# Kernel optimization log

Hardware: AMD Instinct MI355X
Metric: run time of the kernel (lower is better)

Reference implementation:

```python
import jax, jax.numpy as jnp
import numpy as np

N = 100000
E = 1600000
IN_DIM = 512
HID = 64
OUT = 2


def gcn_conv(x, src, dst, W, b, n):
    # transform first (PyG GCNConv: x = x @ W, then propagate)
    xt = x @ W  # [n, d_out]
    # add self-loops
    loop = jnp.arange(n, dtype=src.dtype)
    src_sl = jnp.concatenate([src, loop])
    dst_sl = jnp.concatenate([dst, loop])
    # symmetric normalization: deg over destination (col) incl. self-loops
    ones = jnp.ones(src_sl.shape[0], dtype=xt.dtype)
    deg = jax.ops.segment_sum(ones, dst_sl, num_segments=n)
    dis = jnp.where(deg > 0, jax.lax.rsqrt(deg), 0.0)  # deg^-1/2, inf -> 0
    norm = dis[src_sl] * dis[dst_sl]  # [E+n]
    msgs = xt[src_sl] * norm[:, None]  # gather + scale
    out = jax.ops.segment_sum(msgs, dst_sl, num_segments=n)  # scatter-add
    return out + b


def setup_inputs() -> dict:
    key = jax.random.key(0)
    k0, k1, k2, k3, k4, k5 = jax.random.split(key, 6)
    x = jax.random.normal(k0, (N, IN_DIM), dtype=jnp.float32)
    edge_index = jax.random.randint(k1, (2, E), 0, N, dtype=jnp.int64)
    s1 = 1.0 / np.sqrt(IN_DIM)
    s2 = 1.0 / np.sqrt(HID)
    W1 = jax.random.uniform(k2, (IN_DIM, HID), jnp.float32, -s1, s1)
    b1 = jax.random.uniform(k3, (HID,), jnp.float32, -s1, s1)
    W2 = jax.random.uniform(k4, (HID, OUT), jnp.float32, -s2, s2)
    b2 = jax.random.uniform(k5, (OUT,), jnp.float32, -s2, s2)
    return {"x": x, "edge_index": edge_index, "W1": W1, "b1": b1, "W2": W2, "b2": b2}


def reference(x, edge_index, W1, b1, W2, b2):
    src, dst = edge_index[0], edge_index[1]
    h = gcn_conv(x, src, dst, W1, b1, N)
    h = jax.nn.relu(h)
    # dropout is identity in eval mode (training=False)
    h = gcn_conv(h, src, dst, W2, b2, N)
    return jax.nn.log_softmax(h, axis=1)
```

## Files before the change

### kernel.cpp

```cpp
#include <hip/hip_runtime.h>
#include <hip/hip_bf16.h>

#define NN 100000
#define EE 1600000
#define IN_DIM 512
#define HID 64
#define NB1 391
#define NCH 196
#define CHUNK 8192
#define NGEMM 1563
#define ARENA 5120
#define GA 800
#define GB (NGEMM - GA)

typedef __attribute__((ext_vector_type(8))) short bf16x8;
typedef __attribute__((ext_vector_type(4))) float f32x4;

static __device__ __forceinline__ short f2bf(float f) {
    __hip_bfloat16 h = __float2bfloat16(f);
    return *reinterpret_cast<short*>(&h);
}
static __device__ __forceinline__ float bf2f(unsigned short u) {
    union { unsigned int i; float f; } c; c.i = ((unsigned int)u) << 16;
    return c.f;
}

__device__ __forceinline__ void do_gemm(int gb, const float* __restrict__ x,
                                        const bf16x8* __restrict__ W1p,
                                        unsigned short* __restrict__ xt1b) {
    const int wave = threadIdx.x >> 6;
    const int lane = threadIdx.x & 63;
    const int r = lane & 15;
    const int kg = lane >> 4;
    const int row0 = gb * 64 + wave * 16;
    const int rowc = min(row0 + r, NN - 1);
    const float* xr = x + (size_t)rowc * IN_DIM;

    f32x4 acc[4] = {};
#pragma unroll
    for (int ks = 0; ks < 16; ++ks) {
        const int k0 = ks * 32 + kg * 8;
        float4 xa = *(const float4*)(xr + k0);
        float4 xb = *(const float4*)(xr + k0 + 4);
        bf16x8 a;
        a[0] = f2bf(xa.x); a[1] = f2bf(xa.y); a[2] = f2bf(xa.z); a[3] = f2bf(xa.w);
        a[4] = f2bf(xb.x); a[5] = f2bf(xb.y); a[6] = f2bf(xb.z); a[7] = f2bf(xb.w);
        const int bbase = (ks * 4 + kg) * 64;
#pragma unroll
        for (int cb = 0; cb < 4; ++cb) {
            bf16x8 bfr = W1p[bbase + cb * 16 + r];
            acc[cb] = __builtin_amdgcn_mfma_f32_16x16x32_bf16(a, bfr, acc[cb], 0, 0, 0);
        }
    }
#pragma unroll
    for (int cb = 0; cb < 4; ++cb) {
#pragma unroll
        for (int reg = 0; reg < 4; ++reg) {
            int ro = row0 + kg * 4 + reg;
            if (ro < NN) xt1b[(size_t)ro * HID + cb * 16 + r] =
                (unsigned short)f2bf(acc[cb][reg]);
        }
    }
}

__global__ __launch_bounds__(256) void pack_hist_kernel(const float* __restrict__ W1,
                                                        bf16x8* __restrict__ W1p,
                                                        const int* __restrict__ dst,
                                                        int* __restrict__ cnt2d) {
    if (blockIdx.x < 16) {
        int t = blockIdx.x * 256 + threadIdx.x;
        int kstep = t >> 8;
        int kb = (t >> 6) & 3;
        int col = t & 63;
        int kbase = kstep * 32 + kb * 8;
        bf16x8 v;
#pragma unroll
        for (int j = 0; j < 8; ++j) v[j] = f2bf(W1[(size_t)(kbase + j) * HID + col]);
        W1p[t] = v;
    } else {
        __shared__ int h[NB1];
        const int c = blockIdx.x - 16;
        const int t = threadIdx.x;
        for (int i = t; i < NB1; i += 256) h[i] = 0;
        __syncthreads();
        const int base = c * CHUNK;
        for (int i = t; i < CHUNK; i += 256) {
            int e = base + i;
            if (e < EE) atomicAdd(&h[dst[e] >> 8], 1);
        }
        __syncthreads();
        for (int i = t; i < NB1; i += 256) cnt2d[c * NB1 + i] = h[i];
    }
}

__global__ __launch_bounds__(256) void scatter_gemm_kernel(
        const int* __restrict__ src, const int* __restrict__ dst,
        const int* __restrict__ cnt2d, unsigned int* __restrict__ pairs,
        int* __restrict__ edge_cnt,
        const float* __restrict__ x, const bf16x8* __restrict__ W1p,
        unsigned short* __restrict__ xt1b) {
    if (blockIdx.x < NCH) {
        __shared__ int cur[NB1];
        const int c = blockIdx.x;
        const int t = threadIdx.x;
        for (int i = t; i < NB1; i += 256) {
            int run = 0, pp = 0;
            for (int c2 = 0; c2 < NCH; ++c2) {
                int v = cnt2d[c2 * NB1 + i];
                if (c2 == c) pp = run;
                run += v;
            }
            cur[i] = i * ARENA + pp;
            if (c == 0) edge_cnt[i] = run;
        }
        __syncthreads();
        const int base = c * CHUNK;
        for (int i = t; i < CHUNK; i += 256) {
            int e = base + i;
            if (e < EE) {
                int s = src[e], d = dst[e];
                int bkt = d >> 8;
                int pos = atomicAdd(&cur[bkt], 1);
                if (pos < (bkt + 1) * ARENA)
                    pairs[pos] = ((unsigned int)s << 8) | (unsigned int)(d & 255);
            }
        }
    } else {
        do_gemm(blockIdx.x - NCH, x, W1p, xt1b);
    }
}

__global__ __launch_bounds__(256) void sort_gemm_kernel(
        const unsigned int* __restrict__ pairs, const int* __restrict__ edge_cnt,
        int* __restrict__ offsets, int* __restrict__ cursor,
        int* __restrict__ sorted_src, float* __restrict__ dis,
        const float* __restrict__ x, const bf16x8* __restrict__ W1p,
        unsigned short* __restrict__ xt1b) {
    if (blockIdx.x < NB1) {
        __shared__ int sdeg[256];
        __shared__ int sinc[256];
        __shared__ int scur[256];
        const int b = blockIdx.x;
        const int t = threadIdx.x;
        const int n0 = b << 8;
        const int nn = min(256, NN - n0);
        const int e0 = b * ARENA;
        const int e1 = e0 + min(edge_cnt[b], ARENA);

        sdeg[t] = 0;
        __syncthreads();
        for (int e = e0 + t; e < e1; e += 256)
            atomicAdd(&sdeg[pairs[e] & 255u], 1);
        __syncthreads();
        sinc[t] = sdeg[t];
        __syncthreads();
        for (int off = 1; off < 256; off <<= 1) {
            int v = (t >= off) ? sinc[t - off] : 0;
            __syncthreads();
            sinc[t] += v;
            __syncthreads();
        }
        int excl = sinc[t] - sdeg[t];
        scur[t] = excl;
        if (t < nn) {
            offsets[n0 + t] = e0 + excl;
            cursor[n0 + t]  = e0 + excl + sdeg[t];
            dis[n0 + t]     = rsqrtf((float)sdeg[t] + 1.0f);
        }
        __syncthreads();
        for (int e = e0 + t; e < e1; e += 256) {
            unsigned int p = pairs[e];
            int pos = atomicAdd(&scur[p & 255u], 1);
            sorted_src[e0 + pos] = (int)(p >> 8);
        }
    } else {
        do_gemm(GA + (blockIdx.x - NB1), x, W1p, xt1b);
    }
}

__global__ __launch_bounds__(256) void agg1_fused_kernel(
        const int* __restrict__ offsets, const int* __restrict__ cursor,
        const int* __restrict__ sorted_src, const float* __restrict__ dis,
        const unsigned short* __restrict__ xt1b, const float* __restrict__ b1,
        const float* __restrict__ W2, float* __restrict__ xt2) {
    int node = blockIdx.x * 4 + (threadIdx.x >> 6);
    if (node >= NN) return;
    const int lane = threadIdx.x & 63;
    const int grp = lane >> 4;
    const int fl = lane & 15;
    const int beg = offsets[node], end = cursor[node];
    const float dd = dis[node];
    float acc0 = 0.f, acc1 = 0.f, acc2 = 0.f, acc3 = 0.f;

    for (int base = beg; base < end; base += 64) {
        int m = min(64, end - base);
        int s = 0;
        float nd = 0.f;
        if (lane < m) {
            s = sorted_src[base + lane];
            nd = dis[s];
        }
#pragma unroll 4
        for (int jj = 0; jj < m; jj += 4) {
            int j = jj + grp;
            int sj = __shfl(s, j);
            float nj = __shfl(nd, j);
            float w = (j < m) ? nj : 0.f;
            ushort4 v = *(const ushort4*)(xt1b + (size_t)sj * HID + fl * 4);
            acc0 += bf2f(v.x) * w;
            acc1 += bf2f(v.y) * w;
            acc2 += bf2f(v.z) * w;
            acc3 += bf2f(v.w) * w;
        }
    }
    acc0 += __shfl_xor(acc0, 16); acc0 += __shfl_xor(acc0, 32);
    acc1 += __shfl_xor(acc1, 16); acc1 += __shfl_xor(acc1, 32);
    acc2 += __shfl_xor(acc2, 16); acc2 += __shfl_xor(acc2, 32);
    acc3 += __shfl_xor(acc3, 16); acc3 += __shfl_xor(acc3, 32);

    ushort4 xs = *(const ushort4*)(xt1b + (size_t)node * HID + fl * 4);
    float4 bb = *(const float4*)(b1 + fl * 4);
    float d2 = dd * dd;
    float h0 = fmaxf(acc0 * dd + bf2f(xs.x) * d2 + bb.x, 0.f);
    float h1 = fmaxf(acc1 * dd + bf2f(xs.y) * d2 + bb.y, 0.f);
    float h2 = fmaxf(acc2 * dd + bf2f(xs.z) * d2 + bb.z, 0.f);
    float h3 = fmaxf(acc3 * dd + bf2f(xs.w) * d2 + bb.w, 0.f);

    float4 w01 = *(const float4*)(W2 + fl * 8);
    float4 w23 = *(const float4*)(W2 + fl * 8 + 4);
    float a0 = h0 * w01.x + h1 * w01.z + h2 * w23.x + h3 * w23.z;
    float a1 = h0 * w01.y + h1 * w01.w + h2 * w23.y + h3 * w23.w;
    a0 += __shfl_xor(a0, 1); a0 += __shfl_xor(a0, 2);
    a0 += __shfl_xor(a0, 4); a0 += __shfl_xor(a0, 8);
    a1 += __shfl_xor(a1, 1); a1 += __shfl_xor(a1, 2);
    a1 += __shfl_xor(a1, 4); a1 += __shfl_xor(a1, 8);
    if (lane == 0) *(float2*)(xt2 + (size_t)node * 2) = make_float2(a0, a1);
}

__global__ void agg2_final_kernel(const int* __restrict__ offsets, const int* __restrict__ cursor,
                                  const int* __restrict__ sorted_src,
                                  const float* __restrict__ dis,
                                  const float* __restrict__ xt2,
                                  const float* __restrict__ b2,
                                  float* __restrict__ out) {
    int node = blockIdx.x * 256 + threadIdx.x;
    if (node >= NN) return;
    int beg = offsets[node], end = cursor[node];
    float dd = dis[node];
    float d2 = dd * dd;
    float a0 = xt2[(size_t)node * 2 + 0] * d2;
    float a1 = xt2[(size_t)node * 2 + 1] * d2;
    for (int p = beg; p < end; ++p) {
        int s = sorted_src[p];
        float nrm = dis[s] * dd;
        float2 v = *(const float2*)(xt2 + (size_t)s * 2);
        a0 += v.x * nrm;
        a1 += v.y * nrm;
    }
    float v0 = a0 + b2[0], v1 = a1 + b2[1];
    float m = fmaxf(v0, v1);
    float lse = m + logf(expf(v0 - m) + expf(v1 - m));
    out[(size_t)node * 2 + 0] = v0 - lse;
    out[(size_t)node * 2 + 1] = v1 - lse;
}

extern "C" void kernel_launch(void* const* d_in, const int* in_sizes, int n_in,
                              void* d_out, int out_size, void* d_ws, size_t ws_size,
                              hipStream_t stream) {
    const float* x  = (const float*)d_in[0];
    const int* ei   = (const int*)d_in[1];
    const float* W1 = (const float*)d_in[2];
    const float* b1 = (const float*)d_in[3];
    const float* W2 = (const float*)d_in[4];
    const float* b2 = (const float*)d_in[5];
    const int* src = ei;
    const int* dst = ei + EE;
    float* out = (float*)d_out;

    unsigned short* xt1b = (unsigned short*)d_ws;
    float* dis        = (float*)(xt1b + (size_t)NN * HID);
    int*   offsets    = (int*)(dis + NN);
    int*   cursor     = offsets + NN;
    float* xt2        = (float*)(cursor + NN);
    bf16x8* W1p       = (bf16x8*)(xt2 + (size_t)NN * 2);
    int*   cnt2d      = (int*)(W1p + 4096);
    int*   edge_cnt   = cnt2d + NCH * NB1;
    int*   sorted_src = edge_cnt + NB1;
    unsigned int* pairs = (unsigned int*)(sorted_src + (size_t)NB1 * ARENA);

    pack_hist_kernel<<<16 + NCH, 256, 0, stream>>>(W1, W1p, dst, cnt2d);
    scatter_gemm_kernel<<<NCH + GA, 256, 0, stream>>>(src, dst, cnt2d, pairs, edge_cnt,
                                                      x, W1p, xt1b);
    sort_gemm_kernel<<<NB1 + GB, 256, 0, stream>>>(pairs, edge_cnt, offsets, cursor,
                                                   sorted_src, dis, x, W1p, xt1b);
    agg1_fused_kernel<<<(NN + 3) / 4, 256, 0, stream>>>(offsets, cursor, sorted_src,
                                                        dis, xt1b, b1, W2, xt2);
    agg2_final_kernel<<<(NN + 255) / 256, 256, 0, stream>>>(offsets, cursor, sorted_src,
                                                            dis, xt2, b2, out);
}
```

Baseline: 165.0 us.

## Fold degree normalization into GEMM output and fuse bucket sort with layer-1 aggregation

Result: slower. 322.9 us (+95.7%).

```diff
diff --git a/kernel.cpp b/kernel.cpp
--- a/kernel.cpp
+++ b/kernel.cpp
@@ -10,8 +10,6 @@
 #define CHUNK 8192
 #define NGEMM 1563
 #define ARENA 5120
-#define GA 800
-#define GB (NGEMM - GA)
 
 typedef __attribute__((ext_vector_type(8))) short bf16x8;
 typedef __attribute__((ext_vector_type(4))) float f32x4;
@@ -25,48 +23,11 @@
     return c.f;
 }
 
-__device__ __forceinline__ void do_gemm(int gb, const float* __restrict__ x,
-                                        const bf16x8* __restrict__ W1p,
-                                        unsigned short* __restrict__ xt1b) {
-    const int wave = threadIdx.x >> 6;
-    const int lane = threadIdx.x & 63;
-    const int r = lane & 15;
-    const int kg = lane >> 4;
-    const int row0 = gb * 64 + wave * 16;
-    const int rowc = min(row0 + r, NN - 1);
-    const float* xr = x + (size_t)rowc * IN_DIM;
-
-    f32x4 acc[4] = {};
-#pragma unroll
-    for (int ks = 0; ks < 16; ++ks) {
-        const int k0 = ks * 32 + kg * 8;
-        float4 xa = *(const float4*)(xr + k0);
-        float4 xb = *(const float4*)(xr + k0 + 4);
-        bf16x8 a;
-        a[0] = f2bf(xa.x); a[1] = f2bf(xa.y); a[2] = f2bf(xa.z); a[3] = f2bf(xa.w);
-        a[4] = f2bf(xb.x); a[5] = f2bf(xb.y); a[6] = f2bf(xb.z); a[7] = f2bf(xb.w);
-        const int bbase = (ks * 4 + kg) * 64;
-#pragma unroll
-        for (int cb = 0; cb < 4; ++cb) {
-            bf16x8 bfr = W1p[bbase + cb * 16 + r];
-            acc[cb] = __builtin_amdgcn_mfma_f32_16x16x32_bf16(a, bfr, acc[cb], 0, 0, 0);
-        }
-    }
-#pragma unroll
-    for (int cb = 0; cb < 4; ++cb) {
-#pragma unroll
-        for (int reg = 0; reg < 4; ++reg) {
-            int ro = row0 + kg * 4 + reg;
-            if (ro < NN) xt1b[(size_t)ro * HID + cb * 16 + r] =
-                (unsigned short)f2bf(acc[cb][reg]);
-        }
-    }
-}
-
 __global__ __launch_bounds__(256) void pack_hist_kernel(const float* __restrict__ W1,
                                                         bf16x8* __restrict__ W1p,
                                                         const int* __restrict__ dst,
-                                                        int* __restrict__ cnt2d) {
+                                                        int* __restrict__ cnt2d,
+                                                        int* __restrict__ deg) {
     if (blockIdx.x < 16) {
         int t = blockIdx.x * 256 + threadIdx.x;
         int kstep = t >> 8;
@@ -86,7 +47,11 @@
         const int base = c * CHUNK;
         for (int i = t; i < CHUNK; i += 256) {
             int e = base + i;
-            if (e < EE) atomicAdd(&h[dst[e] >> 8], 1);
+            if (e < EE) {
+                int d = dst[e];
+                atomicAdd(&h[d >> 8], 1);
+                atomicAdd(&deg[d], 1);
+            }
         }
         __syncthreads();
         for (int i = t; i < NB1; i += 256) cnt2d[c * NB1 + i] = h[i];
@@ -98,7 +63,8 @@
         const int* __restrict__ cnt2d, unsigned int* __restrict__ pairs,
         int* __restrict__ edge_cnt,
         const float* __restrict__ x, const bf16x8* __restrict__ W1p,
-        unsigned short* __restrict__ xt1b) {
+        const int* __restrict__ deg, float* __restrict__ dis,
+        unsigned short* __restrict__ y) {
     if (blockIdx.x < NCH) {
         __shared__ int cur[NB1];
         const int c = blockIdx.x;
@@ -126,142 +92,169 @@
             }
         }
     } else {
-        do_gemm(blockIdx.x - NCH, x, W1p, xt1b);
-    }
-}
-
-__global__ __launch_bounds__(256) void sort_gemm_kernel(
+        const int gb = blockIdx.x - NCH;
+        const int wave = threadIdx.x >> 6;
+        const int lane = threadIdx.x & 63;
+        const int r = lane & 15;
+        const int kg = lane >> 4;
+        const int row0 = gb * 64 + wave * 16;
+        const int rowc = min(row0 + r, NN - 1);
+        const float* xr = x + (size_t)rowc * IN_DIM;
+
+        f32x4 acc[4] = {};
+#pragma unroll
+        for (int ks = 0; ks < 16; ++ks) {
+            const int k0 = ks * 32 + kg * 8;
+            float4 xa = *(const float4*)(xr + k0);
+            float4 xb = *(const float4*)(xr + k0 + 4);
+            bf16x8 a;
+            a[0] = f2bf(xa.x); a[1] = f2bf(xa.y); a[2] = f2bf(xa.z); a[3] = f2bf(xa.w);
+            a[4] = f2bf(xb.x); a[5] = f2bf(xb.y); a[6] = f2bf(xb.z); a[7] = f2bf(xb.w);
+            const int bbase = (ks * 4 + kg) * 64;
+#pragma unroll
+            for (int cb = 0; cb < 4; ++cb) {
+                bf16x8 bfr = W1p[bbase + cb * 16 + r];
+                acc[cb] = __builtin_amdgcn_mfma_f32_16x16x32_bf16(a, bfr, acc[cb], 0, 0, 0);
+            }
+        }
+        float di[4];
+#pragma unroll
+        for (int reg = 0; reg < 4; ++reg) {
+            int ro = row0 + kg * 4 + reg;
+            di[reg] = (ro < NN) ? rsqrtf((float)deg[ro] + 1.0f) : 0.f;
+            if (r == 0 && ro < NN) dis[ro] = di[reg];
+        }
+#pragma unroll
+        for (int cb = 0; cb < 4; ++cb) {
+#pragma unroll
+            for (int reg = 0; reg < 4; ++reg) {
+                int ro = row0 + kg * 4 + reg;
+                if (ro < NN) y[(size_t)ro * HID + cb * 16 + r] =
+                    (unsigned short)f2bf(di[reg] * acc[cb][reg]);
+            }
+        }
+    }
+}
+
+__global__ __launch_bounds__(256) void sortagg1_kernel(
         const unsigned int* __restrict__ pairs, const int* __restrict__ edge_cnt,
-        int* __restrict__ offsets, int* __restrict__ cursor,
-        int* __restrict__ sorted_src, float* __restrict__ dis,
-        const float* __restrict__ x, const bf16x8* __restrict__ W1p,
-        unsigned short* __restrict__ xt1b) {
-    if (blockIdx.x < NB1) {
-        __shared__ int sdeg[256];
-        __shared__ int sinc[256];
-        __shared__ int scur[256];
-        const int b = blockIdx.x;
-        const int t = threadIdx.x;
-        const int n0 = b << 8;
-        const int nn = min(256, NN - n0);
-        const int e0 = b * ARENA;
-        const int e1 = e0 + min(edge_cnt[b], ARENA);
-
-        sdeg[t] = 0;
-        __syncthreads();
-        for (int e = e0 + t; e < e1; e += 256)
-            atomicAdd(&sdeg[pairs[e] & 255u], 1);
-        __syncthreads();
-        sinc[t] = sdeg[t];
-        __syncthreads();
-        for (int off = 1; off < 256; off <<= 1) {
-            int v = (t >= off) ? sinc[t - off] : 0;
-            __syncthreads();
-            sinc[t] += v;
-            __syncthreads();
-        }
-        int excl = sinc[t] - sdeg[t];
-        scur[t] = excl;
-        if (t < nn) {
-            offsets[n0 + t] = e0 + excl;
-            cursor[n0 + t]  = e0 + excl + sdeg[t];
-            dis[n0 + t]     = rsqrtf((float)sdeg[t] + 1.0f);
-        }
-        __syncthreads();
-        for (int e = e0 + t; e < e1; e += 256) {
-            unsigned int p = pairs[e];
-            int pos = atomicAdd(&scur[p & 255u], 1);
-            sorted_src[e0 + pos] = (int)(p >> 8);
-        }
-    } else {
-        do_gemm(GA + (blockIdx.x - NB1), x, W1p, xt1b);
-    }
-}
-
-__global__ __launch_bounds__(256) void agg1_fused_kernel(
-        const int* __restrict__ offsets, const int* __restrict__ cursor,
-        const int* __restrict__ sorted_src, const float* __restrict__ dis,
-        const unsigned short* __restrict__ xt1b, const float* __restrict__ b1,
-        const float* __restrict__ W2, float* __restrict__ xt2) {
-    int node = blockIdx.x * 4 + (threadIdx.x >> 6);
-    if (node >= NN) return;
-    const int lane = threadIdx.x & 63;
+        const unsigned short* __restrict__ y, const float* __restrict__ b1,
+        const float* __restrict__ W2, float* __restrict__ z) {
+    __shared__ int lds_src[ARENA];
+    __shared__ int sdeg[256];
+    __shared__ int sinc[256];
+    __shared__ int scur[256];
+    const int b = blockIdx.x;
+    const int t = threadIdx.x;
+    const int n0 = b << 8;
+    const int e0 = b * ARENA;
+    const int cnt = min(edge_cnt[b], ARENA);
+
+    sdeg[t] = 0;
+    __syncthreads();
+    for (int e = t; e < cnt; e += 256)
+        atomicAdd(&sdeg[pairs[e0 + e] & 255u], 1);
+    __syncthreads();
+    sinc[t] = sdeg[t];
+    __syncthreads();
+    for (int off = 1; off < 256; off <<= 1) {
+        int v = (t >= off) ? sinc[t - off] : 0;
+        __syncthreads();
+        sinc[t] += v;
+        __syncthreads();
+    }
+    scur[t] = sinc[t] - sdeg[t];
+    __syncthreads();
+    for (int e = t; e < cnt; e += 256) {
+        unsigned int p = pairs[e0 + e];
+        int pos = atomicAdd(&scur[p & 255u], 1);
+        lds_src[pos] = (int)(p >> 8);
+    }
+    __syncthreads();
+
+    const int w = t >> 6;
+    const int lane = t & 63;
     const int grp = lane >> 4;
     const int fl = lane & 15;
-    const int beg = offsets[node], end = cursor[node];
-    const float dd = dis[node];
-    float acc0 = 0.f, acc1 = 0.f, acc2 = 0.f, acc3 = 0.f;
-
-    for (int base = beg; base < end; base += 64) {
-        int m = min(64, end - base);
-        int s = 0;
-        float nd = 0.f;
-        if (lane < m) {
-            s = sorted_src[base + lane];
-            nd = dis[s];
-        }
-#pragma unroll 4
-        for (int jj = 0; jj < m; jj += 4) {
+    const float4 bb = *(const float4*)(b1 + fl * 4);
+    const float4 w01 = *(const float4*)(W2 + fl * 8);
+    const float4 w23 = *(const float4*)(W2 + fl * 8 + 4);
+
+    for (int i = 0; i < 64; ++i) {
+        int n = w * 64 + i;
+        int node = n0 + n;
+        if (node >= NN) break;
+        int len = sdeg[n];
+        int beg = sinc[n] - len;
+        float dd = rsqrtf((float)len + 1.0f);
+        float acc0 = 0.f, acc1 = 0.f, acc2 = 0.f, acc3 = 0.f;
+        if (grp == 0) {
+            ushort4 v = *(const ushort4*)(y + (size_t)node * HID + fl * 4);
+            acc0 = bf2f(v.x); acc1 = bf2f(v.y); acc2 = bf2f(v.z); acc3 = bf2f(v.w);
+        }
+        for (int jj = 0; jj < len; jj += 4) {
             int j = jj + grp;
-            int sj = __shfl(s, j);
-            float nj = __shfl(nd, j);
-            float w = (j < m) ? nj : 0.f;
-            ushort4 v = *(const ushort4*)(xt1b + (size_t)sj * HID + fl * 4);
-            acc0 += bf2f(v.x) * w;
-            acc1 += bf2f(v.y) * w;
-            acc2 += bf2f(v.z) * w;
-            acc3 += bf2f(v.w) * w;
-        }
-    }
-    acc0 += __shfl_xor(acc0, 16); acc0 += __shfl_xor(acc0, 32);
-    acc1 += __shfl_xor(acc1, 16); acc1 += __shfl_xor(acc1, 32);
-    acc2 += __shfl_xor(acc2, 16); acc2 += __shfl_xor(acc2, 32);
-    acc3 += __shfl_xor(acc3, 16); acc3 += __shfl_xor(acc3, 32);
-
-    ushort4 xs = *(const ushort4*)(xt1b + (size_t)node * HID + fl * 4);
-    float4 bb = *(const float4*)(b1 + fl * 4);
-    float d2 = dd * dd;
-    float h0 = fmaxf(acc0 * dd + bf2f(xs.x) * d2 + bb.x, 0.f);
-    float h1 = fmaxf(acc1 * dd + bf2f(xs.y) * d2 + bb.y, 0.f);
-    float h2 = fmaxf(acc2 * dd + bf2f(xs.z) * d2 + bb.z, 0.f);
-    float h3 = fmaxf(acc3 * dd + bf2f(xs.w) * d2 + bb.w, 0.f);
-
-    float4 w01 = *(const float4*)(W2 + fl * 8);
-    float4 w23 = *(const float4*)(W2 + fl * 8 + 4);
-    float a0 = h0 * w01.x + h1 * w01.z + h2 * w23.x + h3 * w23.z;
-    float a1 = h0 * w01.y + h1 * w01.w + h2 * w23.y + h3 * w23.w;
-    a0 += __shfl_xor(a0, 1); a0 += __shfl_xor(a0, 2);
-    a0 += __shfl_xor(a0, 4); a0 += __shfl_xor(a0, 8);
-    a1 += __shfl_xor(a1, 1); a1 += __shfl_xor(a1, 2);
-    a1 += __shfl_xor(a1, 4); a1 += __shfl_xor(a1, 8);
-    if (lane == 0) *(float2*)(xt2 + (size_t)node * 2) = make_float2(a0, a1);
-}
-
-__global__ void agg2_final_kernel(const int* __restrict__ offsets, const int* __restrict__ cursor,
-                                  const int* __restrict__ sorted_src,
-                                  const float* __restrict__ dis,
-                                  const float* __restrict__ xt2,
-                                  const float* __restrict__ b2,
-                                  float* __restrict__ out) {
-    int node = blockIdx.x * 256 + threadIdx.x;
-    if (node >= NN) return;
-    int beg = offsets[node], end = cursor[node];
-    float dd = dis[node];
-    float d2 = dd * dd;
-    float a0 = xt2[(size_t)node * 2 + 0] * d2;
-    float a1 = xt2[(size_t)node * 2 + 1] * d2;
-    for (int p = beg; p < end; ++p) {
-        int s = sorted_src[p];
-        float nrm = dis[s] * dd;
-        float2 v = *(const float2*)(xt2 + (size_t)s * 2);
-        a0 += v.x * nrm;
-        a1 += v.y * nrm;
-    }
-    float v0 = a0 + b2[0], v1 = a1 + b2[1];
-    float m = fmaxf(v0, v1);
-    float lse = m + logf(expf(v0 - m) + expf(v1 - m));
-    out[(size_t)node * 2 + 0] = v0 - lse;
-    out[(size_t)node * 2 + 1] = v1 - lse;
+            if (j < len) {
+                int s = lds_src[beg + j];
+                ushort4 v = *(const ushort4*)(y + (size_t)s * HID + fl * 4);
+                acc0 += bf2f(v.x);
+                acc1 += bf2f(v.y);
+                acc2 += bf2f(v.z);
+                acc3 += bf2f(v.w);
+            }
+        }
+        acc0 += __shfl_xor(acc0, 16); acc0 += __shfl_xor(acc0, 32);
+        acc1 += __shfl_xor(acc1, 16); acc1 += __shfl_xor(acc1, 32);
+        acc2 += __shfl_xor(acc2, 16); acc2 += __shfl_xor(acc2, 32);
+        acc3 += __shfl_xor(acc3, 16); acc3 += __shfl_xor(acc3, 32);
+
+        float h0 = fmaxf(acc0 * dd + bb.x, 0.f);
+        float h1 = fmaxf(acc1 * dd + bb.y, 0.f);
+        float h2 = fmaxf(acc2 * dd + bb.z, 0.f);
+        float h3 = fmaxf(acc3 * dd + bb.w, 0.f);
+
+        float a0 = h0 * w01.x + h1 * w01.z + h2 * w23.x + h3 * w23.z;
+        float a1 = h0 * w01.y + h1 * w01.w + h2 * w23.y + h3 * w23.w;
+        a0 += __shfl_xor(a0, 1); a0 += __shfl_xor(a0, 2);
+        a0 += __shfl_xor(a0, 4); a0 += __shfl_xor(a0, 8);
+        a1 += __shfl_xor(a1, 1); a1 += __shfl_xor(a1, 2);
+        a1 += __shfl_xor(a1, 4); a1 += __shfl_xor(a1, 8);
+        if (lane == 0) *(float2*)(z + (size_t)node * 2) = make_float2(dd * a0, dd * a1);
+    }
+}
+
+__global__ __launch_bounds__(256) void agg2_kernel(
+        const unsigned int* __restrict__ pairs, const int* __restrict__ edge_cnt,
+        const float* __restrict__ dis, const float* __restrict__ z,
+        const float* __restrict__ b2, float* __restrict__ out) {
+    __shared__ float acc2[256][2];
+    const int b = blockIdx.x;
+    const int t = threadIdx.x;
+    const int n0 = b << 8;
+    const int e0 = b * ARENA;
+    const int cnt = min(edge_cnt[b], ARENA);
+    acc2[t][0] = 0.f; acc2[t][1] = 0.f;
+    __syncthreads();
+    for (int e = t; e < cnt; e += 256) {
+        unsigned int p = pairs[e0 + e];
+        int s = (int)(p >> 8);
+        int dloc = (int)(p & 255u);
+        float2 zv = *(const float2*)(z + (size_t)s * 2);
+        atomicAdd(&acc2[dloc][0], zv.x);
+        atomicAdd(&acc2[dloc][1], zv.y);
+    }
+    __syncthreads();
+    int node = n0 + t;
+    if (node < NN) {
+        float dd = dis[node];
+        float2 zs = *(const float2*)(z + (size_t)node * 2);
+        float v0 = dd * (acc2[t][0] + zs.x) + b2[0];
+        float v1 = dd * (acc2[t][1] + zs.y) + b2[1];
+        float m = fmaxf(v0, v1);
+        float lse = m + logf(expf(v0 - m) + expf(v1 - m));
+        out[(size_t)node * 2 + 0] = v0 - lse;
+        out[(size_t)node * 2 + 1] = v1 - lse;
+    }
 }
 
 extern "C" void kernel_launch(void* const* d_in, const int* in_sizes, int n_in,
@@ -277,24 +270,20 @@
     const int* dst = ei + EE;
     float* out = (float*)d_out;
 
-    unsigned short* xt1b = (unsigned short*)d_ws;
-    float* dis        = (float*)(xt1b + (size_t)NN * HID);
-    int*   offsets    = (int*)(dis + NN);
-    int*   cursor     = offsets + NN;
-    float* xt2        = (float*)(cursor + NN);
-    bf16x8* W1p       = (bf16x8*)(xt2 + (size_t)NN * 2);
+    unsigned short* y = (unsigned short*)d_ws;
+    float* dis        = (float*)(y + (size_t)NN * HID);
+    int*   deg        = (int*)(dis + NN);
+    float* z          = (float*)(deg + NN);
+    bf16x8* W1p       = (bf16x8*)(z + (size_t)NN * 2);
     int*   cnt2d      = (int*)(W1p + 4096);
     int*   edge_cnt   = cnt2d + NCH * NB1;
-    int*   sorted_src = edge_cnt + NB1;
-    unsigned int* pairs = (unsigned int*)(sorted_src + (size_t)NB1 * ARENA);
-
-    pack_hist_kernel<<<16 + NCH, 256, 0, stream>>>(W1, W1p, dst, cnt2d);
-    scatter_gemm_kernel<<<NCH + GA, 256, 0, stream>>>(src, dst, cnt2d, pairs, edge_cnt,
-                                                      x, W1p, xt1b);
-    sort_gemm_kernel<<<NB1 + GB, 256, 0, stream>>>(pairs, edge_cnt, offsets, cursor,
-                                                   sorted_src, dis, x, W1p, xt1b);
-    agg1_fused_kernel<<<(NN + 3) / 4, 256, 0, stream>>>(offsets, cursor, sorted_src,
-                                                        dis, xt1b, b1, W2, xt2);
-    agg2_final_kernel<<<(NN + 255) / 256, 256, 0, stream>>>(offsets, cursor, sorted_src,
-                                                            dis, xt2, b2, out);
-}
+    unsigned int* pairs = (unsigned int*)(edge_cnt + NB1);
+
+    hipMemsetAsync(deg, 0, sizeof(int) * NN, stream);
+
+    pack_hist_kernel<<<16 + NCH, 256, 0, stream>>>(W1, W1p, dst, cnt2d, deg);
+    scatter_gemm_kernel<<<NCH + NGEMM, 256, 0, stream>>>(src, dst, cnt2d, pairs, edge_cnt,
+                                                         x, W1p, deg, dis, y);
+    sortagg1_kernel<<<NB1, 256, 0, stream>>>(pairs, edge_cnt, y, b1, W2, z);
+    agg2_kernel<<<NB1, 256, 0, stream>>>(pairs, edge_cnt, dis, z, b2, out);
+}
```

## Prescale GEMM rows by source degree norm to drop per-edge dis gathers

Applied to the files above, without the earlier changes.

Result: slower. 225.1 us (+36.4%).

```diff
diff --git a/kernel.cpp b/kernel.cpp
--- a/kernel.cpp
+++ b/kernel.cpp
@@ -27,7 +27,9 @@
 
 __device__ __forceinline__ void do_gemm(int gb, const float* __restrict__ x,
                                         const bf16x8* __restrict__ W1p,
-                                        unsigned short* __restrict__ xt1b) {
+                                        const int* __restrict__ deg,
+                                        float* __restrict__ dis,
+                                        unsigned short* __restrict__ y) {
     const int wave = threadIdx.x >> 6;
     const int lane = threadIdx.x & 63;
     const int r = lane & 15;
@@ -52,13 +54,20 @@
             acc[cb] = __builtin_amdgcn_mfma_f32_16x16x32_bf16(a, bfr, acc[cb], 0, 0, 0);
         }
     }
+    float di[4];
+#pragma unroll
+    for (int reg = 0; reg < 4; ++reg) {
+        int ro = row0 + kg * 4 + reg;
+        di[reg] = (ro < NN) ? rsqrtf((float)deg[ro] + 1.0f) : 0.f;
+        if (r == 0 && ro < NN) dis[ro] = di[reg];
+    }
 #pragma unroll
     for (int cb = 0; cb < 4; ++cb) {
 #pragma unroll
         for (int reg = 0; reg < 4; ++reg) {
             int ro = row0 + kg * 4 + reg;
-            if (ro < NN) xt1b[(size_t)ro * HID + cb * 16 + r] =
-                (unsigned short)f2bf(acc[cb][reg]);
+            if (ro < NN) y[(size_t)ro * HID + cb * 16 + r] =
+                (unsigned short)f2bf(di[reg] * acc[cb][reg]);
         }
     }
 }
@@ -66,7 +75,8 @@
 __global__ __launch_bounds__(256) void pack_hist_kernel(const float* __restrict__ W1,
                                                         bf16x8* __restrict__ W1p,
                                                         const int* __restrict__ dst,
-                                                        int* __restrict__ cnt2d) {
+                                                        int* __restrict__ cnt2d,
+                                                        int* __restrict__ deg) {
     if (blockIdx.x < 16) {
         int t = blockIdx.x * 256 + threadIdx.x;
         int kstep = t >> 8;
@@ -86,7 +96,11 @@
         const int base = c * CHUNK;
         for (int i = t; i < CHUNK; i += 256) {
             int e = base + i;
-            if (e < EE) atomicAdd(&h[dst[e] >> 8], 1);
+            if (e < EE) {
+                int d = dst[e];
+                atomicAdd(&h[d >> 8], 1);
+                atomicAdd(&deg[d], 1);
+            }
         }
         __syncthreads();
         for (int i = t; i < NB1; i += 256) cnt2d[c * NB1 + i] = h[i];
@@ -98,7 +112,8 @@
         const int* __restrict__ cnt2d, unsigned int* __restrict__ pairs,
         int* __restrict__ edge_cnt,
         const float* __restrict__ x, const bf16x8* __restrict__ W1p,
-        unsigned short* __restrict__ xt1b) {
+        const int* __restrict__ deg, float* __restrict__ dis,
+        unsigned short* __restrict__ y) {
     if (blockIdx.x < NCH) {
         __shared__ int cur[NB1];
         const int c = blockIdx.x;
@@ -126,16 +141,17 @@
             }
         }
     } else {
-        do_gemm(blockIdx.x - NCH, x, W1p, xt1b);
+        do_gemm(blockIdx.x - NCH, x, W1p, deg, dis, y);
     }
 }
 
 __global__ __launch_bounds__(256) void sort_gemm_kernel(
         const unsigned int* __restrict__ pairs, const int* __restrict__ edge_cnt,
         int* __restrict__ offsets, int* __restrict__ cursor,
-        int* __restrict__ sorted_src, float* __restrict__ dis,
+        int* __restrict__ sorted_src,
         const float* __restrict__ x, const bf16x8* __restrict__ W1p,
-        unsigned short* __restrict__ xt1b) {
+        const int* __restrict__ deg, float* __restrict__ dis,
+        unsigned short* __restrict__ y) {
     if (blockIdx.x < NB1) {
         __shared__ int sdeg[256];
         __shared__ int sinc[256];
@@ -165,7 +181,6 @@
         if (t < nn) {
             offsets[n0 + t] = e0 + excl;
             cursor[n0 + t]  = e0 + excl + sdeg[t];
-            dis[n0 + t]     = rsqrtf((float)sdeg[t] + 1.0f);
         }
         __syncthreads();
         for (int e = e0 + t; e < e1; e += 256) {
@@ -174,90 +189,92 @@
             sorted_src[e0 + pos] = (int)(p >> 8);
         }
     } else {
-        do_gemm(GA + (blockIdx.x - NB1), x, W1p, xt1b);
+        do_gemm(GA + (blockIdx.x - NB1), x, W1p, deg, dis, y);
     }
 }
 
 __global__ __launch_bounds__(256) void agg1_fused_kernel(
         const int* __restrict__ offsets, const int* __restrict__ cursor,
-        const int* __restrict__ sorted_src, const float* __restrict__ dis,
-        const unsigned short* __restrict__ xt1b, const float* __restrict__ b1,
-        const float* __restrict__ W2, float* __restrict__ xt2) {
+        const int* __restrict__ sorted_src, const unsigned short* __restrict__ y,
+        const float* __restrict__ dis, const float* __restrict__ b1,
+        const float* __restrict__ W2, float* __restrict__ z) {
     int node = blockIdx.x * 4 + (threadIdx.x >> 6);
     if (node >= NN) return;
     const int lane = threadIdx.x & 63;
-    const int grp = lane >> 4;
-    const int fl = lane & 15;
+    const int grp = lane >> 3;
+    const int fl = lane & 7;
     const int beg = offsets[node], end = cursor[node];
     const float dd = dis[node];
-    float acc0 = 0.f, acc1 = 0.f, acc2 = 0.f, acc3 = 0.f;
-
+    float acc[8] = {};
+
+    if (grp == 0) {
+        bf16x8 v = *(const bf16x8*)(y + (size_t)node * HID + fl * 8);
+#pragma unroll
+        for (int k = 0; k < 8; ++k) acc[k] = bf2f((unsigned short)v[k]);
+    }
     for (int base = beg; base < end; base += 64) {
         int m = min(64, end - base);
         int s = 0;
-        float nd = 0.f;
-        if (lane < m) {
-            s = sorted_src[base + lane];
-            nd = dis[s];
-        }
-#pragma unroll 4
-        for (int jj = 0; jj < m; jj += 4) {
+        if (lane < m) s = sorted_src[base + lane];
+#pragma unroll 2
+        for (int jj = 0; jj < m; jj += 8) {
             int j = jj + grp;
-            int sj = __shfl(s, j);
-            float nj = __shfl(nd, j);
-            float w = (j < m) ? nj : 0.f;
-            ushort4 v = *(const ushort4*)(xt1b + (size_t)sj * HID + fl * 4);
-            acc0 += bf2f(v.x) * w;
-            acc1 += bf2f(v.y) * w;
-            acc2 += bf2f(v.z) * w;
-            acc3 += bf2f(v.w) * w;
-        }
-    }
-    acc0 += __shfl_xor(acc0, 16); acc0 += __shfl_xor(acc0, 32);
-    acc1 += __shfl_xor(acc1, 16); acc1 += __shfl_xor(acc1, 32);
-    acc2 += __shfl_xor(acc2, 16); acc2 += __shfl_xor(acc2, 32);
-    acc3 += __shfl_xor(acc3, 16); acc3 += __shfl_xor(acc3, 32);
-
-    ushort4 xs = *(const ushort4*)(xt1b + (size_t)node * HID + fl * 4);
-    float4 bb = *(const float4*)(b1 + fl * 4);
-    float d2 = dd * dd;
-    float h0 = fmaxf(acc0 * dd + bf2f(xs.x) * d2 + bb.x, 0.f);
-    float h1 = fmaxf(acc1 * dd + bf2f(xs.y) * d2 + bb.y, 0.f);
-    float h2 = fmaxf(acc2 * dd + bf2f(xs.z) * d2 + bb.z, 0.f);
-    float h3 = fmaxf(acc3 * dd + bf2f(xs.w) * d2 + bb.w, 0.f);
-
-    float4 w01 = *(const float4*)(W2 + fl * 8);
-    float4 w23 = *(const float4*)(W2 + fl * 8 + 4);
-    float a0 = h0 * w01.x + h1 * w01.z + h2 * w23.x + h3 * w23.z;
-    float a1 = h0 * w01.y + h1 * w01.w + h2 * w23.y + h3 * w23.w;
-    a0 += __shfl_xor(a0, 1); a0 += __shfl_xor(a0, 2);
-    a0 += __shfl_xor(a0, 4); a0 += __shfl_xor(a0, 8);
-    a1 += __shfl_xor(a1, 1); a1 += __shfl_xor(a1, 2);
-    a1 += __shfl_xor(a1, 4); a1 += __shfl_xor(a1, 8);
-    if (lane == 0) *(float2*)(xt2 + (size_t)node * 2) = make_float2(a0, a1);
+            if (j < m) {
+                int sj = __shfl(s, j);
+                bf16x8 v = *(const bf16x8*)(y + (size_t)sj * HID + fl * 8);
+#pragma unroll
+                for (int k = 0; k < 8; ++k) acc[k] += bf2f((unsigned short)v[k]);
+            }
+        }
+    }
+#pragma unroll
+    for (int k = 0; k < 8; ++k) {
+        acc[k] += __shfl_xor(acc[k], 8);
+        acc[k] += __shfl_xor(acc[k], 16);
+        acc[k] += __shfl_xor(acc[k], 32);
+    }
+    float4 b_lo = *(const float4*)(b1 + fl * 8);
+    float4 b_hi = *(const float4*)(b1 + fl * 8 + 4);
+    float4 w0 = *(const float4*)(W2 + fl * 16);
+    float4 w1 = *(const float4*)(W2 + fl * 16 + 4);
+    float4 w2 = *(const float4*)(W2 + fl * 16 + 8);
+    float4 w3 = *(const float4*)(W2 + fl * 16 + 12);
+    float h0 = fmaxf(dd * acc[0] + b_lo.x, 0.f);
+    float h1 = fmaxf(dd * acc[1] + b_lo.y, 0.f);
+    float h2 = fmaxf(dd * acc[2] + b_lo.z, 0.f);
+    float h3 = fmaxf(dd * acc[3] + b_lo.w, 0.f);
+    float h4 = fmaxf(dd * acc[4] + b_hi.x, 0.f);
+    float h5 = fmaxf(dd * acc[5] + b_hi.y, 0.f);
+    float h6 = fmaxf(dd * acc[6] + b_hi.z, 0.f);
+    float h7 = fmaxf(dd * acc[7] + b_hi.w, 0.f);
+    float a0 = h0 * w0.x + h1 * w0.z + h2 * w1.x + h3 * w1.z
+             + h4 * w2.x + h5 * w2.z + h6 * w3.x + h7 * w3.z;
+    float a1 = h0 * w0.y + h1 * w0.w + h2 * w1.y + h3 * w1.w
+             + h4 * w2.y + h5 * w2.w + h6 * w3.y + h7 * w3.w;
+    a0 += __shfl_xor(a0, 1); a0 += __shfl_xor(a0, 2); a0 += __shfl_xor(a0, 4);
+    a1 += __shfl_xor(a1, 1); a1 += __shfl_xor(a1, 2); a1 += __shfl_xor(a1, 4);
+    if (lane == 0) *(float2*)(z + (size_t)node * 2) = make_float2(dd * a0, dd * a1);
 }
 
 __global__ void agg2_final_kernel(const int* __restrict__ offsets, const int* __restrict__ cursor,
                                   const int* __restrict__ sorted_src,
                                   const float* __restrict__ dis,
-                                  const float* __restrict__ xt2,
+                                  const float* __restrict__ z,
                                   const float* __restrict__ b2,
                                   float* __restrict__ out) {
     int node = blockIdx.x * 256 + threadIdx.x;
     if (node >= NN) return;
     int beg = offsets[node], end = cursor[node];
     float dd = dis[node];
-    float d2 = dd * dd;
-    float a0 = xt2[(size_t)node * 2 + 0] * d2;
-    float a1 = xt2[(size_t)node * 2 + 1] * d2;
+    float2 zs = *(const float2*)(z + (size_t)node * 2);
+    float a0 = zs.x, a1 = zs.y;
     for (int p = beg; p < end; ++p) {
         int s = sorted_src[p];
-        float nrm = dis[s] * dd;
-        float2 v = *(const float2*)(xt2 + (size_t)s * 2);
-        a0 += v.x * nrm;
-        a1 += v.y * nrm;
-    }
-    float v0 = a0 + b2[0], v1 = a1 + b2[1];
+        float2 v = *(const float2*)(z + (size_t)s * 2);
+        a0 += v.x;
+        a1 += v.y;
+    }
+    float v0 = dd * a0 + b2[0], v1 = dd * a1 + b2[1];
     float m = fmaxf(v0, v1);
     float lse = m + logf(expf(v0 - m) + expf(v1 - m));
     out[(size_t)node * 2 + 0] = v0 - lse;
@@ -277,24 +294,27 @@
     const int* dst = ei + EE;
     float* out = (float*)d_out;
 
-    unsigned short* xt1b = (unsigned short*)d_ws;
-    float* dis        = (float*)(xt1b + (size_t)NN * HID);
-    int*   offsets    = (int*)(dis + NN);
+    unsigned short* y = (unsigned short*)d_ws;
+    float* dis        = (float*)(y + (size_t)NN * HID);
+    int*   deg        = (int*)(dis + NN);
+    int*   offsets    = deg + NN;
     int*   cursor     = offsets + NN;
-    float* xt2        = (float*)(cursor + NN);
-    bf16x8* W1p       = (bf16x8*)(xt2 + (size_t)NN * 2);
+    float* z          = (float*)(cursor + NN);
+    bf16x8* W1p       = (bf16x8*)(z + (size_t)NN * 2);
     int*   cnt2d      = (int*)(W1p + 4096);
     int*   edge_cnt   = cnt2d + NCH * NB1;
     int*   sorted_src = edge_cnt + NB1;
     unsigned int* pairs = (unsigned int*)(sorted_src + (size_t)NB1 * ARENA);
 
-    pack_hist_kernel<<<16 + NCH, 256, 0, stream>>>(W1, W1p, dst, cnt2d);
+    hipMemsetAsync(deg, 0, sizeof(int) * NN, stream);
+
+    pack_hist_kernel<<<16 + NCH, 256, 0, stream>>>(W1, W1p, dst, cnt2d, deg);
     scatter_gemm_kernel<<<NCH + GA, 256, 0, stream>>>(src, dst, cnt2d, pairs, edge_cnt,
-                                                      x, W1p, xt1b);
+                                                      x, W1p, deg, dis, y);
     sort_gemm_kernel<<<NB1 + GB, 256, 0, stream>>>(pairs, edge_cnt, offsets, cursor,
-                                                   sorted_src, dis, x, W1p, xt1b);
+                                                   sorted_src, x, W1p, deg, dis, y);
     agg1_fused_kernel<<<(NN + 3) / 4, 256, 0, stream>>>(offsets, cursor, sorted_src,
-                                                        dis, xt1b, b1, W2, xt2);
+                                                        y, dis, b1, W2, z);
     agg2_final_kernel<<<(NN + 255) / 256, 256, 0, stream>>>(offsets, cursor, sorted_src,
-                                                            dis, xt2, b2, out);
-}
+                                                            dis, z, b2, out);
+}
```

## Split W1 packing into its own kernel and overlap GEMM with histogram

Applied to the files above, without the earlier changes.

Result: slower. 169.4 us (+2.7%).

```diff
diff --git a/kernel.cpp b/kernel.cpp
--- a/kernel.cpp
+++ b/kernel.cpp
@@ -10,8 +10,9 @@
 #define CHUNK 8192
 #define NGEMM 1563
 #define ARENA 5120
-#define GA 800
-#define GB (NGEMM - GA)
+#define GH 400
+#define GA 650
+#define GB (NGEMM - GH - GA)
 
 typedef __attribute__((ext_vector_type(8))) short bf16x8;
 typedef __attribute__((ext_vector_type(4))) float f32x4;
@@ -25,9 +26,22 @@
     return c.f;
 }
 
+__global__ __launch_bounds__(256) void pack_kernel(const float* __restrict__ W1,
+                                                   bf16x8* __restrict__ W1p) {
+    int t = blockIdx.x * 256 + threadIdx.x;
+    int kstep = t >> 8;
+    int kb = (t >> 6) & 3;
+    int col = t & 63;
+    int kbase = kstep * 32 + kb * 8;
+    bf16x8 v;
+#pragma unroll
+    for (int j = 0; j < 8; ++j) v[j] = f2bf(W1[(size_t)(kbase + j) * HID + col]);
+    W1p[t] = v;
+}
+
 __device__ __forceinline__ void do_gemm(int gb, const float* __restrict__ x,
                                         const bf16x8* __restrict__ W1p,
-                                        unsigned short* __restrict__ xt1b) {
+                                        unsigned short* __restrict__ y) {
     const int wave = threadIdx.x >> 6;
     const int lane = threadIdx.x & 63;
     const int r = lane & 15;
@@ -57,29 +71,20 @@
 #pragma unroll
         for (int reg = 0; reg < 4; ++reg) {
             int ro = row0 + kg * 4 + reg;
-            if (ro < NN) xt1b[(size_t)ro * HID + cb * 16 + r] =
+            if (ro < NN) y[(size_t)ro * HID + cb * 16 + r] =
                 (unsigned short)f2bf(acc[cb][reg]);
         }
     }
 }
 
-__global__ __launch_bounds__(256) void pack_hist_kernel(const float* __restrict__ W1,
-                                                        bf16x8* __restrict__ W1p,
-                                                        const int* __restrict__ dst,
-                                                        int* __restrict__ cnt2d) {
-    if (blockIdx.x < 16) {
-        int t = blockIdx.x * 256 + threadIdx.x;
-        int kstep = t >> 8;
-        int kb = (t >> 6) & 3;
-        int col = t & 63;
-        int kbase = kstep * 32 + kb * 8;
-        bf16x8 v;
-#pragma unroll
-        for (int j = 0; j < 8; ++j) v[j] = f2bf(W1[(size_t)(kbase + j) * HID + col]);
-        W1p[t] = v;
-    } else {
+__global__ __launch_bounds__(256) void hist_gemm_kernel(const int* __restrict__ dst,
+                                                        int* __restrict__ cnt2d,
+                                                        const float* __restrict__ x,
+                                                        const bf16x8* __restrict__ W1p,
+                                                        unsigned short* __restrict__ y) {
+    if (blockIdx.x < NCH) {
         __shared__ int h[NB1];
-        const int c = blockIdx.x - 16;
+        const int c = blockIdx.x;
         const int t = threadIdx.x;
         for (int i = t; i < NB1; i += 256) h[i] = 0;
         __syncthreads();
@@ -90,6 +95,8 @@
         }
         __syncthreads();
         for (int i = t; i < NB1; i += 256) cnt2d[c * NB1 + i] = h[i];
+    } else {
+        do_gemm(blockIdx.x - NCH, x, W1p, y);
     }
 }
 
@@ -98,7 +105,7 @@
         const int* __restrict__ cnt2d, unsigned int* __restrict__ pairs,
         int* __restrict__ edge_cnt,
         const float* __restrict__ x, const bf16x8* __restrict__ W1p,
-        unsigned short* __restrict__ xt1b) {
+        unsigned short* __restrict__ y) {
     if (blockIdx.x < NCH) {
         __shared__ int cur[NB1];
         const int c = blockIdx.x;
@@ -126,7 +133,7 @@
             }
         }
     } else {
-        do_gemm(blockIdx.x - NCH, x, W1p, xt1b);
+        do_gemm(GH + (blockIdx.x - NCH), x, W1p, y);
     }
 }
 
@@ -135,7 +142,7 @@
         int* __restrict__ offsets, int* __restrict__ cursor,
         int* __restrict__ sorted_src, float* __restrict__ dis,
         const float* __restrict__ x, const bf16x8* __restrict__ W1p,
-        unsigned short* __restrict__ xt1b) {
+        unsigned short* __restrict__ y) {
     if (blockIdx.x < NB1) {
         __shared__ int sdeg[256];
         __shared__ int sinc[256];
@@ -174,14 +181,14 @@
             sorted_src[e0 + pos] = (int)(p >> 8);
         }
     } else {
-        do_gemm(GA + (blockIdx.x - NB1), x, W1p, xt1b);
+        do_gemm(GH + GA + (blockIdx.x - NB1), x, W1p, y);
     }
 }
 
 __global__ __launch_bounds__(256) void agg1_fused_kernel(
         const int* __restrict__ offsets, const int* __restrict__ cursor,
         const int* __restrict__ sorted_src, const float* __restrict__ dis,
-        const unsigned short* __restrict__ xt1b, const float* __restrict__ b1,
+        const unsigned short* __restrict__ y, const float* __restrict__ b1,
         const float* __restrict__ W2, float* __restrict__ xt2) {
     int node = blockIdx.x * 4 + (threadIdx.x >> 6);
     if (node >= NN) return;
@@ -206,7 +213,7 @@
             int sj = __shfl(s, j);
             float nj = __shfl(nd, j);
             float w = (j < m) ? nj : 0.f;
-            ushort4 v = *(const ushort4*)(xt1b + (size_t)sj * HID + fl * 4);
+            ushort4 v = *(const ushort4*)(y + (size_t)sj * HID + fl * 4);
             acc0 += bf2f(v.x) * w;
             acc1 += bf2f(v.y) * w;
             acc2 += bf2f(v.z) * w;
@@ -218,7 +225,7 @@
     acc2 += __shfl_xor(acc2, 16); acc2 += __shfl_xor(acc2, 32);
     acc3 += __shfl_xor(acc3, 16); acc3 += __shfl_xor(acc3, 32);
 
-    ushort4 xs = *(const ushort4*)(xt1b + (size_t)node * HID + fl * 4);
+    ushort4 xs = *(const ushort4*)(y + (size_t)node * HID + fl * 4);
     float4 bb = *(const float4*)(b1 + fl * 4);
     float d2 = dd * dd;
     float h0 = fmaxf(acc0 * dd + bf2f(xs.x) * d2 + bb.x, 0.f);
@@ -277,8 +284,8 @@
     const int* dst = ei + EE;
     float* out = (float*)d_out;
 
-    unsigned short* xt1b = (unsigned short*)d_ws;
-    float* dis        = (float*)(xt1b + (size_t)NN * HID);
+    unsigned short* y = (unsigned short*)d_ws;
+    float* dis        = (float*)(y + (size_t)NN * HID);
     int*   offsets    = (int*)(dis + NN);
     int*   cursor     = offsets + NN;
     float* xt2        = (float*)(cursor + NN);
@@ -288,13 +295,14 @@
     int*   sorted_src = edge_cnt + NB1;
     unsigned int* pairs = (unsigned int*)(sorted_src + (size_t)NB1 * ARENA);
 
-    pack_hist_kernel<<<16 + NCH, 256, 0, stream>>>(W1, W1p, dst, cnt2d);
+    pack_kernel<<<16, 256, 0, stream>>>(W1, W1p);
+    hist_gemm_kernel<<<NCH + GH, 256, 0, stream>>>(dst, cnt2d, x, W1p, y);
     scatter_gemm_kernel<<<NCH + GA, 256, 0, stream>>>(src, dst, cnt2d, pairs, edge_cnt,
-                                                      x, W1p, xt1b);
+                                                      x, W1p, y);
     sort_gemm_kernel<<<NB1 + GB, 256, 0, stream>>>(pairs, edge_cnt, offsets, cursor,
-                                                   sorted_src, dis, x, W1p, xt1b);
+                                                   sorted_src, dis, x, W1p, y);
     agg1_fused_kernel<<<(NN + 3) / 4, 256, 0, stream>>>(offsets, cursor, sorted_src,
-                                                        dis, xt1b, b1, W2, xt2);
+                                                        dis, y, b1, W2, xt2);
     agg2_final_kernel<<<(NN + 255) / 256, 256, 0, stream>>>(offsets, cursor, sorted_src,
                                                             dis, xt2, b2, out);
 }
```
